# Kernel tuning notes

Hardware: AMD Instinct MI355X
Metric: run time of the kernel (lower is better)

Reference implementation:

```python
import jax, jax.numpy as jnp
import numpy as np

D, H, DH, FF, L = 1024, 8, 128, 2048, 3
TEXT_V, UNIT_V = 128257, 10001
LN_EPS = 1e-5
TEMP = 0.0005
NEG = -1e9


def _layer_norm(x, s, b):
    m = x.mean(-1, keepdims=True)
    v = ((x - m) ** 2).mean(-1, keepdims=True)
    return (x - m) / jnp.sqrt(v + LN_EPS) * s + b


def _encoder(tokens, pad_idx, emb, ipw, ipb, ow, ob, l1s, l1b, f1w, f1b, f2w, f2b, l2s, l2b):
    pad = tokens == pad_idx  # [B,S] key padding mask
    x = emb[tokens]  # [B,S,D]; padding row of emb is zero
    B, S, _ = x.shape
    scale = 1.0 / np.sqrt(DH).astype(np.float32)
    for l in range(L):
        # --- self attention (post-norm, PyTorch TransformerEncoderLayer default) ---
        qkv = x @ ipw[l].T + ipb[l]  # [B,S,3D]
        q, k, v = jnp.split(qkv, 3, axis=-1)
        q = q.reshape(B, S, H, DH)
        k = k.reshape(B, S, H, DH)
        v = v.reshape(B, S, H, DH)
        scores = jnp.einsum('bqhd,bkhd->bhqk', q, k) * scale
        scores = jnp.where(pad[:, None, None, :], NEG, scores)
        attn = jax.nn.softmax(scores, axis=-1)
        o = jnp.einsum('bhqk,bkhd->bqhd', attn, v).reshape(B, S, D)
        o = o @ ow[l].T + ob[l]
        x = _layer_norm(x + o, l1s[l], l1b[l])
        # --- feedforward ---
        ff = jax.nn.relu(x @ f1w[l].T + f1b[l]) @ f2w[l].T + f2b[l]
        x = _layer_norm(x + ff, l2s[l], l2b[l])
    return x, pad


def _enc_params(key, V):
    ks = jax.random.split(key, 4)
    emb = jax.random.normal(ks[0], (V, D), jnp.float32) * 0.02
    emb = emb.at[V - 1].set(0.0)  # padding_idx row is zero
    return dict(
        emb=emb,
        ipw=jax.random.normal(ks[1], (L, 3 * D, D), jnp.float32) * 0.02,
        ipb=jnp.zeros((L, 3 * D), jnp.float32),
        ow=jax.random.normal(ks[2], (L, D, D), jnp.float32) * 0.02,
        ob=jnp.zeros((L, D), jnp.float32),
        l1s=jnp.ones((L, D), jnp.float32),
        l1b=jnp.zeros((L, D), jnp.float32),
        f1w=jax.random.normal(ks[3], (L, FF, D), jnp.float32) * 0.02,
        f1b=jnp.zeros((L, FF), jnp.float32),
        f2w=jax.random.normal(jax.random.fold_in(ks[3], 1), (L, D, FF), jnp.float32) * 0.02,
        f2b=jnp.zeros((L, D), jnp.float32),
        l2s=jnp.ones((L, D), jnp.float32),
        l2b=jnp.zeros((L, D), jnp.float32),
    )


def setup_inputs() -> dict:
    key = jax.random.key(0)
    k_tt, k_ut, k_tp, k_up = jax.random.split(key, 4)
    B, T, U = 8, 256, 1024
    inp = {
        'text_tokens': jax.random.randint(k_tt, (B, T), 0, TEXT_V - 1, jnp.int32),
        'unit_tokens': jax.random.randint(k_ut, (B, U), 0, UNIT_V - 1, jnp.int32),
    }
    for name, p in _enc_params(k_tp, TEXT_V).items():
        inp['t_' + name] = p
    for name, p in _enc_params(k_up, UNIT_V).items():
        inp['u_' + name] = p
    return inp


def reference(text_tokens, unit_tokens,
              t_emb, t_ipw, t_ipb, t_ow, t_ob, t_l1s, t_l1b, t_f1w, t_f1b, t_f2w, t_f2b, t_l2s, t_l2b,
              u_emb, u_ipw, u_ipb, u_ow, u_ob, u_l1s, u_l1b, u_f1w, u_f1b, u_f2w, u_f2b, u_l2s, u_l2b):
    tf, tpad = _encoder(text_tokens, TEXT_V - 1, t_emb, t_ipw, t_ipb, t_ow, t_ob,
                        t_l1s, t_l1b, t_f1w, t_f1b, t_f2w, t_f2b, t_l2s, t_l2b)
    uf, upad = _encoder(unit_tokens, UNIT_V - 1, u_emb, u_ipw, u_ipb, u_ow, u_ob,
                        u_l1s, u_l1b, u_f1w, u_f1b, u_f2w, u_f2b, u_l2s, u_l2b)
    # squared L2 distance via |a-b|^2 = |a|^2 + |b|^2 - 2 a.b (avoids [B,U,T,D] tensor)
    un = jnp.sum(uf * uf, axis=-1)  # [B,U]
    tn = jnp.sum(tf * tf, axis=-1)  # [B,T]
    cross = jnp.einsum('bud,btd->but', uf, tf)  # [B,U,T]
    dist = -TEMP * (un[:, :, None] + tn[:, None, :] - 2.0 * cross)
    mask = upad[:, :, None] | tpad[:, None, :]
    filled = jnp.where(mask, NEG, dist)
    return jax.nn.log_softmax(filled, axis=-1)  # [B,U,T]
```

## Files before the change

### kernel.cpp

```cpp
#include <hip/hip_runtime.h>
#include <stdint.h>

typedef _Float16 half_t;
typedef _Float16 half8 __attribute__((ext_vector_type(8)));
typedef float floatx4 __attribute__((ext_vector_type(4)));

#define D_MODEL 1024
#define NHEAD 8
#define DHEAD 128
#define FF_DIM 2048
#define NLAYER 3
#define BATCH 8
#define TSEQ 256
#define USEQ 1024
#define TPAD 128256
#define UPAD 10000
#define TEMP_ 5e-4f
#define SCALE_QK 0.08838834764831845f

__device__ inline float blk_sum(float v, float* sh) {
#pragma unroll
  for (int o = 32; o; o >>= 1) v += __shfl_xor(v, o, 64);
  __syncthreads();
  if ((threadIdx.x & 63) == 0) sh[threadIdx.x >> 6] = v;
  __syncthreads();
  return sh[0] + sh[1] + sh[2] + sh[3];
}
__device__ inline float blk_max(float v, float* sh) {
#pragma unroll
  for (int o = 32; o; o >>= 1) v = fmaxf(v, __shfl_xor(v, o, 64));
  __syncthreads();
  if ((threadIdx.x & 63) == 0) sh[threadIdx.x >> 6] = v;
  __syncthreads();
  return fmaxf(fmaxf(sh[0], sh[1]), fmaxf(sh[2], sh[3]));
}

__global__ __launch_bounds__(256)
void gemm_bt_kernel(const half_t* __restrict__ A, long lda, long sAb, long sAz,
                    const half_t* __restrict__ B, long ldb, long sBb, long sBz,
                    float* __restrict__ Cf, half_t* __restrict__ Ch,
                    long ldc, long sCb, long sCz,
                    const float* __restrict__ bias,
                    int M, int N, int K, float alpha, int relu, int zdiv) {
  __shared__ __align__(16) half_t As[128 * 64];
  __shared__ __align__(16) half_t Bs[128 * 64];

  const int z = blockIdx.z;
  const int zb = z / zdiv, zh = z % zdiv;
  A += (long)zb * sAb + (long)zh * sAz;
  B += (long)zb * sBb + (long)zh * sBz;
  const long coff = (long)zb * sCb + (long)zh * sCz;

  const int tid = threadIdx.x;
  const int lane = tid & 63;
  const int wid = tid >> 6;
  const long row0 = (long)blockIdx.y * 128;
  const long col0 = (long)blockIdx.x * 128;

  const int srow = tid >> 3;
  const int sg = tid & 7;

  const int wm = (wid & 1) << 6;
  const int wn = (wid >> 1) << 6;
  const int fm = lane & 15;
  const int quad = lane >> 4;

  floatx4 acc[4][4] = {};

  for (int k0 = 0; k0 < K; k0 += 64) {
#pragma unroll
    for (int i = 0; i < 4; ++i) {
      const int r = srow + (i << 5);
      const int gsw = (sg ^ (r & 7)) << 3;
      uint4 va = *(const uint4*)(A + (row0 + r) * lda + k0 + (sg << 3));
      *(uint4*)(&As[(r << 6) + gsw]) = va;
      uint4 vb = *(const uint4*)(B + (col0 + r) * ldb + k0 + (sg << 3));
      *(uint4*)(&Bs[(r << 6) + gsw]) = vb;
    }
    __syncthreads();
#pragma unroll
    for (int kk = 0; kk < 64; kk += 32) {
      const int gq = (kk >> 3) + quad;
      half8 af[4], bfr[4];
#pragma unroll
      for (int mi = 0; mi < 4; ++mi) {
        const int r = wm + (mi << 4) + fm;
        af[mi] = *(const half8*)(&As[(r << 6) + ((gq ^ (r & 7)) << 3)]);
      }
#pragma unroll
      for (int ni = 0; ni < 4; ++ni) {
        const int r = wn + (ni << 4) + fm;
        bfr[ni] = *(const half8*)(&Bs[(r << 6) + ((gq ^ (r & 7)) << 3)]);
      }
#pragma unroll
      for (int mi = 0; mi < 4; ++mi)
#pragma unroll
        for (int ni = 0; ni < 4; ++ni)
          acc[mi][ni] = __builtin_amdgcn_mfma_f32_16x16x32_f16(af[mi], bfr[ni], acc[mi][ni], 0, 0, 0);
    }
    __syncthreads();
  }

#pragma unroll
  for (int ni = 0; ni < 4; ++ni) {
    const long col = col0 + wn + (ni << 4) + fm;
    const float bv = bias ? bias[col] : 0.0f;
#pragma unroll
    for (int mi = 0; mi < 4; ++mi) {
#pragma unroll
      for (int r = 0; r < 4; ++r) {
        const long row = row0 + wm + (mi << 4) + (quad << 2) + r;
        float v = acc[mi][ni][r] * alpha + bv;
        if (relu) v = fmaxf(v, 0.0f);
        const long idx = coff + row * ldc + col;
        if (Cf) Cf[idx] = v;
        if (Ch) Ch[idx] = (half_t)v;
      }
    }
  }
}

__global__ void cvt_kernel(const float* __restrict__ in, half_t* __restrict__ out, long n) {
  long i = (long)blockIdx.x * 256 + threadIdx.x;
  const long stride = (long)gridDim.x * 256;
  for (; i < n; i += stride) out[i] = (half_t)in[i];
}

__global__ __launch_bounds__(256) void embed_kernel(const int* __restrict__ tok,
                                                    const float* __restrict__ emb,
                                                    float* __restrict__ xf, half_t* __restrict__ xh) {
  const long r = blockIdx.x;
  const long src = (long)tok[r] * D_MODEL;
  for (int j = threadIdx.x; j < D_MODEL; j += 256) {
    const float v = emb[src + j];
    xf[r * D_MODEL + j] = v;
    xh[r * D_MODEL + j] = (half_t)v;
  }
}

__global__ __launch_bounds__(256) void ln_kernel(float* x, const float* y,
                                                 const float* s, const float* b, half_t* xh) {
  const int row = blockIdx.x, tid = threadIdx.x;
  float* xr = x + (long)row * D_MODEL;
  const float* yr = y + (long)row * D_MODEL;
  float v[4], sum = 0.f, sq = 0.f;
#pragma unroll
  for (int c = 0; c < 4; ++c) {
    const int j = tid + (c << 8);
    const float t = xr[j] + yr[j];
    v[c] = t; sum += t; sq += t * t;
  }
  __shared__ float sh[4];
  sum = blk_sum(sum, sh);
  sq = blk_sum(sq, sh);
  const float mean = sum * (1.0f / D_MODEL);
  const float var = sq * (1.0f / D_MODEL) - mean * mean;
  const float inv = rsqrtf(var + 1e-5f);
#pragma unroll
  for (int c = 0; c < 4; ++c) {
    const int j = tid + (c << 8);
    const float t = (v[c] - mean) * inv * s[j] + b[j];
    xr[j] = t;
    xh[(long)row * D_MODEL + j] = (half_t)t;
  }
}

__global__ __launch_bounds__(256) void softmax_kernel(half_t* sc, const int* __restrict__ tok,
                                                      int S, int padidx) {
  const int q = blockIdx.x, z = blockIdx.y;
  const int b = z >> 3;
  half_t* row = sc + (long)z * S * S + (long)q * S;
  const int* tb = tok + (long)b * S;
  const int nc = S >> 8;
  const int tid = threadIdx.x;
  float v[4];
  float m = -3e38f;
  for (int c = 0; c < nc; ++c) {
    const int j = tid + (c << 8);
    float x = (float)row[j];
    if (tb[j] == padidx) x = -1e9f;
    v[c] = x;
    m = fmaxf(m, x);
  }
  __shared__ float sh[4];
  m = blk_max(m, sh);
  float ssum = 0.f;
  for (int c = 0; c < nc; ++c) { v[c] = expf(v[c] - m); ssum += v[c]; }
  ssum = blk_sum(ssum, sh);
  const float inv = 1.0f / ssum;
  for (int c = 0; c < nc; ++c) row[tid + (c << 8)] = (half_t)(v[c] * inv);
}

__global__ __launch_bounds__(256) void vtrans_kernel(const half_t* __restrict__ qkv,
                                                     half_t* __restrict__ vt, int S) {
  __shared__ half_t tile[64][65];
  const int s0 = blockIdx.x * 64, d0 = blockIdx.y * 64, z = blockIdx.z;
  const int b = z >> 3, h = z & 7;
  const half_t* src = qkv + (long)b * S * (3 * D_MODEL) + 2 * D_MODEL + h * DHEAD;
  for (int idx = threadIdx.x; idx < 4096; idx += 256) {
    const int r = idx >> 6, c = idx & 63;
    tile[r][c] = src[(long)(s0 + r) * (3 * D_MODEL) + d0 + c];
  }
  __syncthreads();
  half_t* dst = vt + ((long)z * DHEAD + d0) * S + s0;
  for (int idx = threadIdx.x; idx < 4096; idx += 256) {
    const int r = idx >> 6, c = idx & 63;
    dst[(long)r * S + c] = tile[c][r];
  }
}

__global__ __launch_bounds__(256) void rowsq_kernel(const float* __restrict__ x, float* __restrict__ o) {
  const int row = blockIdx.x, tid = threadIdx.x;
  const float* xr = x + (long)row * D_MODEL;
  float s = 0.f;
#pragma unroll
  for (int c = 0; c < 4; ++c) { const float t = xr[tid + (c << 8)]; s += t * t; }
  __shared__ float sh[4];
  s = blk_sum(s, sh);
  if (tid == 0) o[row] = s;
}

__global__ __launch_bounds__(256) void dist_lsm_kernel(float* out, const float* __restrict__ un,
                                                       const float* __restrict__ tn,
                                                       const int* __restrict__ utok,
                                                       const int* __restrict__ ttok) {
  const int u = blockIdx.x, b = blockIdx.y, t = threadIdx.x;
  const long off = ((long)(b * USEQ + u)) * TSEQ;
  const float c = out[off + t];
  float x = -TEMP_ * (un[b * USEQ + u] + tn[b * TSEQ + t] - 2.0f * c);
  if (utok[b * USEQ + u] == UPAD || ttok[b * TSEQ + t] == TPAD) x = -1e9f;
  __shared__ float sh[4];
  const float m = blk_max(x, sh);
  const float e = expf(x - m);
  const float s = blk_sum(e, sh);
  out[off + t] = x - m - logf(s);
}

static void launch_gemm(hipStream_t st, const half_t* A, long lda, long sAb, long sAz,
                        const half_t* B, long ldb, long sBb, long sBz,
                        float* Cf, half_t* Ch, long ldc, long sCb, long sCz,
                        const float* bias, int M, int N, int K, float alpha, int relu,
                        int zdiv, int nz) {
  dim3 g(N / 128, M / 128, nz), blk(256);
  gemm_bt_kernel<<<g, blk, 0, st>>>(A, lda, sAb, sAz, B, ldb, sBb, sBz,
                                    Cf, Ch, ldc, sCb, sCz, bias, M, N, K, alpha, relu, zdiv);
}

struct EncW {
  const int* tok; int S;
  const float *emb, *ipb, *ob, *l1s, *l1b, *f1b, *f2b, *l2s, *l2b;
  const half_t *ipw, *ow, *f1w, *f2w;
  int padidx;
};
struct Bufs {
  float *xf, *yf;
  half_t *xh, *qkv, *vt, *sc, *oh, *ffh;
};

static void run_encoder(hipStream_t st, const EncW& w, const Bufs& bb) {
  const int S = w.S, Ntok = BATCH * S;
  embed_kernel<<<Ntok, 256, 0, st>>>(w.tok, w.emb, bb.xf, bb.xh);
  for (int l = 0; l < NLAYER; ++l) {
    launch_gemm(st, bb.xh, D_MODEL, 0, 0,
                w.ipw + (size_t)l * 3 * D_MODEL * D_MODEL, D_MODEL, 0, 0,
                nullptr, bb.qkv, 3 * D_MODEL, 0, 0,
                w.ipb + (size_t)l * 3 * D_MODEL, Ntok, 3 * D_MODEL, D_MODEL, 1.0f, 0, 1, 1);
    vtrans_kernel<<<dim3(S / 64, DHEAD / 64, BATCH * NHEAD), 256, 0, st>>>(bb.qkv, bb.vt, S);
    launch_gemm(st, bb.qkv, 3 * D_MODEL, (long)S * 3 * D_MODEL, DHEAD,
                bb.qkv + D_MODEL, 3 * D_MODEL, (long)S * 3 * D_MODEL, DHEAD,
                nullptr, bb.sc, S, (long)NHEAD * S * S, (long)S * S,
                nullptr, S, S, DHEAD, SCALE_QK, 0, NHEAD, BATCH * NHEAD);
    softmax_kernel<<<dim3(S, BATCH * NHEAD), 256, 0, st>>>(bb.sc, w.tok, S, w.padidx);
    launch_gemm(st, bb.sc, S, (long)NHEAD * S * S, (long)S * S,
                bb.vt, S, (long)NHEAD * DHEAD * S, (long)DHEAD * S,
                nullptr, bb.oh, D_MODEL, (long)S * D_MODEL, DHEAD,
                nullptr, S, DHEAD, S, 1.0f, 0, NHEAD, BATCH * NHEAD);
    launch_gemm(st, bb.oh, D_MODEL, 0, 0,
                w.ow + (size_t)l * D_MODEL * D_MODEL, D_MODEL, 0, 0,
                bb.yf, nullptr, D_MODEL, 0, 0,
                w.ob + (size_t)l * D_MODEL, Ntok, D_MODEL, D_MODEL, 1.0f, 0, 1, 1);
    ln_kernel<<<Ntok, 256, 0, st>>>(bb.xf, bb.yf, w.l1s + (size_t)l * D_MODEL,
                                    w.l1b + (size_t)l * D_MODEL, bb.xh);
    launch_gemm(st, bb.xh, D_MODEL, 0, 0,
                w.f1w + (size_t)l * FF_DIM * D_MODEL, D_MODEL, 0, 0,
                nullptr, bb.ffh, FF_DIM, 0, 0,
                w.f1b + (size_t)l * FF_DIM, Ntok, FF_DIM, D_MODEL, 1.0f, 1, 1, 1);
    launch_gemm(st, bb.ffh, FF_DIM, 0, 0,
                w.f2w + (size_t)l * D_MODEL * FF_DIM, FF_DIM, 0, 0,
                bb.yf, nullptr, D_MODEL, 0, 0,
                w.f2b + (size_t)l * D_MODEL, Ntok, D_MODEL, FF_DIM, 1.0f, 0, 1, 1);
    ln_kernel<<<Ntok, 256, 0, st>>>(bb.xf, bb.yf, w.l2s + (size_t)l * D_MODEL,
                                    w.l2b + (size_t)l * D_MODEL, bb.xh);
  }
}

extern "C" void kernel_launch(void* const* d_in, const int* in_sizes, int n_in,
                              void* d_out, int out_size, void* d_ws, size_t ws_size,
                              hipStream_t stream) {
  (void)in_sizes; (void)n_in; (void)out_size; (void)ws_size;
  const int* ttok = (const int*)d_in[0];
  const int* utok = (const int*)d_in[1];
  const float* tp[13];
  const float* up[13];
  for (int i = 0; i < 13; ++i) tp[i] = (const float*)d_in[2 + i];
  for (int i = 0; i < 13; ++i) up[i] = (const float*)d_in[15 + i];

  char* wp = (char*)d_ws;
  auto alloc = [&](size_t bytes) {
    void* p = wp;
    wp += (bytes + 255) & ~(size_t)255;
    return p;
  };
  const size_t IPW = (size_t)NLAYER * 3 * D_MODEL * D_MODEL;
  const size_t OW = (size_t)NLAYER * D_MODEL * D_MODEL;
  const size_t F1W = (size_t)NLAYER * FF_DIM * D_MODEL;
  const size_t F2W = (size_t)NLAYER * D_MODEL * FF_DIM;
  half_t* t_ipw = (half_t*)alloc(IPW * 2);
  half_t* t_ow = (half_t*)alloc(OW * 2);
  half_t* t_f1w = (half_t*)alloc(F1W * 2);
  half_t* t_f2w = (half_t*)alloc(F2W * 2);
  half_t* u_ipw = (half_t*)alloc(IPW * 2);
  half_t* u_ow = (half_t*)alloc(OW * 2);
  half_t* u_f1w = (half_t*)alloc(F1W * 2);
  half_t* u_f2w = (half_t*)alloc(F2W * 2);
  Bufs bb;
  bb.xf = (float*)alloc((size_t)BATCH * USEQ * D_MODEL * 4);
  bb.yf = (float*)alloc((size_t)BATCH * USEQ * D_MODEL * 4);
  bb.xh = (half_t*)alloc((size_t)BATCH * USEQ * D_MODEL * 2);
  bb.qkv = (half_t*)alloc((size_t)BATCH * USEQ * 3 * D_MODEL * 2);
  bb.vt = (half_t*)alloc((size_t)BATCH * NHEAD * DHEAD * USEQ * 2);
  bb.sc = (half_t*)alloc((size_t)BATCH * NHEAD * USEQ * USEQ * 2);
  bb.oh = (half_t*)alloc((size_t)BATCH * USEQ * D_MODEL * 2);
  bb.ffh = (half_t*)alloc((size_t)BATCH * USEQ * FF_DIM * 2);
  half_t* tfh = (half_t*)alloc((size_t)BATCH * TSEQ * D_MODEL * 2);
  float* tn = (float*)alloc((size_t)BATCH * TSEQ * 4);
  float* un = (float*)alloc((size_t)BATCH * USEQ * 4);

  cvt_kernel<<<2048, 256, 0, stream>>>(tp[1], t_ipw, (long)IPW);
  cvt_kernel<<<2048, 256, 0, stream>>>(tp[3], t_ow, (long)OW);
  cvt_kernel<<<2048, 256, 0, stream>>>(tp[7], t_f1w, (long)F1W);
  cvt_kernel<<<2048, 256, 0, stream>>>(tp[9], t_f2w, (long)F2W);
  cvt_kernel<<<2048, 256, 0, stream>>>(up[1], u_ipw, (long)IPW);
  cvt_kernel<<<2048, 256, 0, stream>>>(up[3], u_ow, (long)OW);
  cvt_kernel<<<2048, 256, 0, stream>>>(up[7], u_f1w, (long)F1W);
  cvt_kernel<<<2048, 256, 0, stream>>>(up[9], u_f2w, (long)F2W);

  EncW tw{ttok, TSEQ, tp[0], tp[2], tp[4], tp[5], tp[6], tp[8], tp[10], tp[11], tp[12],
          t_ipw, t_ow, t_f1w, t_f2w, TPAD};
  run_encoder(stream, tw, bb);
  rowsq_kernel<<<BATCH * TSEQ, 256, 0, stream>>>(bb.xf, tn);
  hipMemcpyAsync(tfh, bb.xh, (size_t)BATCH * TSEQ * D_MODEL * 2, hipMemcpyDeviceToDevice, stream);

  EncW uw{utok, USEQ, up[0], up[2], up[4], up[5], up[6], up[8], up[10], up[11], up[12],
          u_ipw, u_ow, u_f1w, u_f2w, UPAD};
  run_encoder(stream, uw, bb);
  rowsq_kernel<<<BATCH * USEQ, 256, 0, stream>>>(bb.xf, un);

  float* out = (float*)d_out;
  launch_gemm(stream, bb.xh, D_MODEL, (long)USEQ * D_MODEL, 0,
              tfh, D_MODEL, (long)TSEQ * D_MODEL, 0,
              out, nullptr, TSEQ, (long)USEQ * TSEQ, 0,
              nullptr, USEQ, TSEQ, D_MODEL, 1.0f, 0, 1, BATCH);
  dist_lsm_kernel<<<dim3(USEQ, BATCH), 256, 0, stream>>>(out, un, tn, utok, ttok);
}
```

Baseline: 2.931 ms.

## Add 256x256 tiled GEMM with direct-to-LDS loads and phased pipelining

Adds a second GEMM kernel that uses 256x256 output tiles with 512 threads. It loads global data straight into LDS through global_load_lds, double-buffers the K loop in four quadrant phases with fine-grained vmcnt waits, raises wave priority around the MFMA blocks, and remaps workgroups with an XCD-aware swizzle. The dispatcher uses it only when M and N are multiples of 256 and the grid has at least 128 tiles; otherwise the old 128x128 kernel runs. The aim is more operand reuse and better overlap of memory and compute on the large encoder GEMMs. The costs are 128KB of LDS per workgroup and fewer workgroups on the smaller shapes.

```diff
diff --git a/kernel.cpp b/kernel.cpp
--- a/kernel.cpp
+++ b/kernel.cpp
@@ -118,6 +118,136 @@
       }
     }
   }
+}
+
+typedef const __attribute__((address_space(1))) uint32_t* gas1_u32;
+typedef __attribute__((address_space(3))) uint32_t* las3_u32;
+__device__ __forceinline__ void gload16(const half_t* g, half_t* l) {
+  __builtin_amdgcn_global_load_lds((gas1_u32)g, (las3_u32)l, 16, 0, 0);
+}
+#define VMW(n) asm volatile("s_waitcnt vmcnt(" #n ")" ::: "memory")
+
+#define STAGE(dst, src, ld, roff, kc)                                          \
+  {                                                                            \
+    _Pragma("unroll") for (int j_ = 0; j_ < 2; ++j_) {                         \
+      const int rb_ = (j_ << 6) + (wid << 3);                                  \
+      const int rr_ = rb_ + (lane >> 3);                                       \
+      const int gg_ = (lane & 7) ^ (rr_ & 7);                                  \
+      gload16((src) + ((long)(roff) + rr_) * (ld) + (kc) + (gg_ << 3),         \
+              (dst) + (rb_ << 6));                                             \
+    }                                                                          \
+  }
+
+#define PHASE(aa, bb, STG, WT)                                                 \
+  {                                                                            \
+    half8 af0_[4], af1_[4], bf0_[2], bf1_[2];                                  \
+    _Pragma("unroll") for (int mi = 0; mi < 4; ++mi) {                         \
+      const int r_ = (wr << 6) + (mi << 4) + fm;                               \
+      half_t* ap_ = &As[d][aa][(r_ << 6)];                                     \
+      af0_[mi] = *(const half8*)(ap_ + ((quad ^ (r_ & 7)) << 3));              \
+      af1_[mi] = *(const half8*)(ap_ + (((4 + quad) ^ (r_ & 7)) << 3));        \
+    }                                                                          \
+    _Pragma("unroll") for (int ni = 0; ni < 2; ++ni) {                         \
+      const int r_ = (wc << 5) + (ni << 4) + fm;                               \
+      half_t* bp_ = &Bs[d][bb][(r_ << 6)];                                     \
+      bf0_[ni] = *(const half8*)(bp_ + ((quad ^ (r_ & 7)) << 3));              \
+      bf1_[ni] = *(const half8*)(bp_ + (((4 + quad) ^ (r_ & 7)) << 3));        \
+    }                                                                          \
+    STG;                                                                       \
+    __builtin_amdgcn_s_barrier();                                              \
+    __builtin_amdgcn_s_setprio(1);                                             \
+    _Pragma("unroll") for (int mi = 0; mi < 4; ++mi)                           \
+      _Pragma("unroll") for (int ni = 0; ni < 2; ++ni) {                       \
+        acc[aa][bb][mi][ni] = __builtin_amdgcn_mfma_f32_16x16x32_f16(          \
+            af0_[mi], bf0_[ni], acc[aa][bb][mi][ni], 0, 0, 0);                 \
+        acc[aa][bb][mi][ni] = __builtin_amdgcn_mfma_f32_16x16x32_f16(          \
+            af1_[mi], bf1_[ni], acc[aa][bb][mi][ni], 0, 0, 0);                 \
+      }                                                                        \
+    __builtin_amdgcn_s_setprio(0);                                             \
+    WT;                                                                        \
+    __builtin_amdgcn_s_barrier();                                              \
+  }
+
+__global__ __launch_bounds__(512, 2)
+void gemm256_kernel(const half_t* __restrict__ A, long lda, long sAb, long sAz,
+                    const half_t* __restrict__ B, long ldb, long sBb, long sBz,
+                    float* __restrict__ Cf, half_t* __restrict__ Ch,
+                    long ldc, long sCb, long sCz,
+                    const float* __restrict__ bias,
+                    int M, int N, int K, float alpha, int relu, int zdiv) {
+  __shared__ __align__(16) half_t As[2][2][128 * 64];
+  __shared__ __align__(16) half_t Bs[2][2][128 * 64];
+
+  const int z = blockIdx.z;
+  const int zb = z / zdiv, zh = z % zdiv;
+  A += (long)zb * sAb + (long)zh * sAz;
+  B += (long)zb * sBb + (long)zh * sBz;
+  const long coff = (long)zb * sCb + (long)zh * sCz;
+
+  const int gx = (int)gridDim.x;
+  const int nwg = gx * (int)gridDim.y;
+  const int orig = (int)blockIdx.y * gx + (int)blockIdx.x;
+  const int q_ = nwg >> 3, r_ = nwg & 7, x_ = orig & 7, i_ = orig >> 3;
+  const int swz = (x_ < r_ ? x_ * (q_ + 1) : r_ * (q_ + 1) + (x_ - r_) * q_) + i_;
+  const long row0 = (long)(swz / gx) * 256;
+  const long col0 = (long)(swz % gx) * 256;
+
+  const int tid = threadIdx.x;
+  const int lane = tid & 63;
+  const int wid = tid >> 6;
+  const int wr = wid >> 2;
+  const int wc = wid & 3;
+  const int fm = lane & 15;
+  const int quad = lane >> 4;
+
+  floatx4 acc[2][2][4][2] = {};
+  const int NT = K >> 6;
+
+  STAGE(&As[0][0][0], A, lda, row0, 0);
+  STAGE(&Bs[0][0][0], B, ldb, col0, 0);
+  STAGE(&Bs[0][1][0], B, ldb, col0 + 128, 0);
+  STAGE(&As[0][1][0], A, lda, row0 + 128, 0);
+  VMW(4);
+  __builtin_amdgcn_s_barrier();
+
+  for (int t = 0; t < NT; ++t) {
+    const int d = t & 1, e = d ^ 1;
+    const int kn = (t + 1) << 6;
+    if (t + 1 < NT) {
+      PHASE(0, 0,
+            { STAGE(&As[e][0][0], A, lda, row0, kn); STAGE(&Bs[e][0][0], B, ldb, col0, kn); },
+            VMW(6));
+      PHASE(0, 1, { STAGE(&Bs[e][1][0], B, ldb, col0 + 128, kn); }, VMW(6));
+      PHASE(1, 0, { STAGE(&As[e][1][0], A, lda, row0 + 128, kn); }, ;);
+      PHASE(1, 1, ;, VMW(4));
+    } else {
+      PHASE(0, 0, ;, VMW(2));
+      PHASE(0, 1, ;, VMW(0));
+      PHASE(1, 0, ;, ;);
+      PHASE(1, 1, ;, ;);
+    }
+  }
+
+#pragma unroll
+  for (int a2 = 0; a2 < 2; ++a2)
+#pragma unroll
+    for (int b2 = 0; b2 < 2; ++b2)
+#pragma unroll
+      for (int ni = 0; ni < 2; ++ni) {
+        const long col = col0 + (b2 << 7) + (wc << 5) + (ni << 4) + fm;
+        const float bv = bias ? bias[col] : 0.0f;
+#pragma unroll
+        for (int mi = 0; mi < 4; ++mi)
+#pragma unroll
+          for (int r = 0; r < 4; ++r) {
+            const long row = row0 + (a2 << 7) + (wr << 6) + (mi << 4) + (quad << 2) + r;
+            float v = acc[a2][b2][mi][ni][r] * alpha + bv;
+            if (relu) v = fmaxf(v, 0.0f);
+            const long idx = coff + row * ldc + col;
+            if (Cf) Cf[idx] = v;
+            if (Ch) Ch[idx] = (half_t)v;
+          }
+      }
 }
 
 __global__ void cvt_kernel(const float* __restrict__ in, half_t* __restrict__ out, long n) {
@@ -241,9 +371,16 @@
                         float* Cf, half_t* Ch, long ldc, long sCb, long sCz,
                         const float* bias, int M, int N, int K, float alpha, int relu,
                         int zdiv, int nz) {
-  dim3 g(N / 128, M / 128, nz), blk(256);
-  gemm_bt_kernel<<<g, blk, 0, st>>>(A, lda, sAb, sAz, B, ldb, sBb, sBz,
-                                    Cf, Ch, ldc, sCb, sCz, bias, M, N, K, alpha, relu, zdiv);
+  const long nb256 = ((M & 255) || (N & 255)) ? 0 : (long)(M / 256) * (N / 256) * nz;
+  if (nb256 >= 128) {
+    dim3 g(N / 256, M / 256, nz), blk(512);
+    gemm256_kernel<<<g, blk, 0, st>>>(A, lda, sAb, sAz, B, ldb, sBb, sBz,
+                                      Cf, Ch, ldc, sCb, sCz, bias, M, N, K, alpha, relu, zdiv);
+  } else {
+    dim3 g(N / 128, M / 128, nz), blk(256);
+    gemm_bt_kernel<<<g, blk, 0, st>>>(A, lda, sAb, sAz, B, ldb, sBb, sBz,
+                                      Cf, Ch, ldc, sCb, sCz, bias, M, N, K, alpha, relu, zdiv);
+  }
 }
 
 struct EncW {
```

Result: slower. 5.056 ms (+72.5%).
